# Kernel optimization log

Hardware: AMD Instinct MI355X
Metric: run time of the kernel (lower is better)

## Reference

```python
import jax, jax.numpy as jnp
import numpy as np

NUM_SEGMENTS = 128  # number of graphs (index.max()+1)


def setup_inputs() -> dict:
    key = jax.random.key(0)
    k1, k2, k3 = jax.random.split(key, 3)
    N, F, T, S, B = 200000, 3, 32, 32, NUM_SEGMENTS
    x = jax.random.normal(k1, (N, F), dtype=jnp.float32)
    v = jax.random.normal(k2, (F, T), dtype=jnp.float32)
    # lin exactly as in the module: linspace(-r, r, bump_steps).view(-1,1,1)
    lin = jnp.linspace(-1.1, 1.1, S, dtype=jnp.float32).reshape(S, 1, 1)
    index = jnp.sort(jax.random.randint(k3, (N,), 0, B, dtype=jnp.int64))
    return {"x": x, "index": index, "v": v, "lin": lin, "scale": 500}


def reference(x, index, v, lin, scale):
    # nh: node heights [N, T]
    nh = x @ v
    # ecc: [S, N, T] broadcasted sigmoid bump
    ecc = jax.nn.sigmoid(scale * (lin - nh))
    # scatter-add over nodes into per-graph bins, then movedim(0,1):
    # segment_sum over leading axis after transposing to [N, S, T]
    # gives [B, S, T] directly (== index_add over dim 1 then movedim).
    out = jax.ops.segment_sum(jnp.transpose(ecc, (1, 0, 2)), index,
                              num_segments=NUM_SEGMENTS)
    return out
```

## Files before the change

kernel.cpp:

```cpp
#include <hip/hip_runtime.h>

#define NSEG 128
#define SSTEPS 32
#define TDIM 32
#define NG 8
#define DROWS 35
#define SPB 8
#define CSTR (DROWS * TDIM)
#define THREADS 256

__global__ __launch_bounds__(THREADS) void ect_kernel(
    const float* __restrict__ x,
    const int*   __restrict__ idx,
    const float* __restrict__ v,
    const float* __restrict__ lin,
    const int*   __restrict__ scale_p,
    float*       __restrict__ out,
    int N)
{
    __shared__ float d[NG][DROWS][TDIM];
    __shared__ float4 xs[NG][32];
    __shared__ int s_bounds[2];

    const int tid = threadIdx.x;
    const unsigned bx = blockIdx.x;
    const int b = bx >> 3;
    const int j = bx & (SPB - 1);

    if (tid < 64) {
        const int L = tid & 31;
        const int h = tid >> 5;
        const int target = b + h;
        const int g0 = (int)(((long long)target * N) >> 7);

        const int hi_last = idx[N - 1];
        int p1 = g0 - 1024 + 64 * L;
        int pc1 = min(max(p1, 0), N - 1);
        int val32 = idx[pc1];
        const bool is64 = (hi_last == 0);
        int val = is64 ? idx[2 * pc1] : val32;

        bool pred1 = (p1 < 0) ? true : ((p1 >= N) ? false : (val < target));
        unsigned long long m1 = __ballot(pred1);
        unsigned hm1 = (unsigned)(m1 >> (h * 32));

        if (hm1 == 0u || hm1 == 0xFFFFFFFFu) {
            if (L == 0) {
                int lo = 0, hi = N;
                while (lo < hi) {
                    int mid = (lo + hi) >> 1;
                    int vv = is64 ? idx[2 * mid] : idx[mid];
                    if (vv < target) lo = mid + 1; else hi = mid;
                }
                s_bounds[h] = lo;
            }
        } else {
            const int A = g0 - 1024 + 64 * (31 - __builtin_clz(hm1));
            int p2 = A + 1 + 2 * L;
            int pc2 = min(max(p2, 0), N - 1);
            int v2 = is64 ? idx[2 * pc2] : idx[pc2];
            bool pred2 = (p2 < 0) ? true : ((p2 >= N) ? false : (v2 < target));
            unsigned long long m2 = __ballot(pred2);
            unsigned hm2 = (unsigned)(m2 >> (h * 32));
            const int B = hm2 ? (A + 1 + 2 * (31 - __builtin_clz(hm2))) : A;
            int p3 = B + 1;
            int pc3 = min(p3, N - 1);
            int v3 = is64 ? idx[2 * pc3] : idx[pc3];
            bool pred3 = (p3 >= N) ? false : (v3 < target);
            if (L == 0) s_bounds[h] = pred3 ? (B + 2) : (B + 1);
        }
    } else {
        float4* dz = (float4*)d;
        for (int i = tid - 64; i < NG * CSTR / 4; i += THREADS - 64)
            dz[i] = make_float4(0.f, 0.f, 0.f, 0.f);
    }

    const float lin0 = lin[0];
    const float step = lin[1] - lin0;
    const float inv_step = 1.0f / step;
    const float negl0 = -lin0 * inv_step;
    const float scale = (float)scale_p[0];
    const float zstep = scale * step;

    const int t = tid & 31;
    const int g = tid >> 5;
    const float v0 = v[t], v1 = v[TDIM + t], v2 = v[2 * TDIM + t];
    float* dg = &d[g][0][t];

    __syncthreads();

    const int start = s_bounds[0], end = s_bounds[1];
    const int cnt_n = end - start;
    const int chunk = (cnt_n + SPB - 1) / SPB;
    const int k0 = start + j * chunk;
    const int k1 = min(k0 + chunk, end);

    {
        const int span = k1 - k0;
        const int cg = (span > 0) ? ((span + NG - 1) >> 3) : 0;
        const int kg0 = k0 + g * cg;
        const int kg1 = min(kg0 + cg, k1);
        float4* xsg = &xs[g][0];
        float cnt = 0.f;

        for (int kb = kg0; kb < kg1; kb += 32) {
            const int nb = min(32, kg1 - kb);
            if (t < nb) {
                const float* xp = x + (size_t)(kb + t) * 3;
                xsg[t] = make_float4(xp[0], xp[1], xp[2], 0.f);
            }
            float4 cur = xsg[0];
            for (int r = 0; r < nb; ++r) {
                const float4 nxt = xsg[min(r + 1, nb - 1)];

                const float nh = fmaf(cur.x, v0, fmaf(cur.y, v1, cur.z * v2));
                float u = fmaf(nh, inv_step, negl0);
                u = fminf(fmaxf(u, -2.0f), 34.0f);
                const float rf = rintf(u);
                if (rf < 32.0f) {
                    if (rf <= -2.0f) cnt += 1.0f;
                    else {
                        const float E = __expf((rf - u) * zstep);
                        const float a = E * __builtin_amdgcn_rcpf(1.0f + E);
                        const int row = (int)rf + 2;
                        float* p = dg + row * 32;
                        const float a0 = p[0];
                        const float a1 = p[32];
                        p[0]  = a0 + a;
                        p[32] = a1 + (1.0f - a);
                    }
                }
                cur = nxt;
            }
        }
        dg[0] = cnt;
    }
    __syncthreads();

    {
        float4* c0 = (float4*)d;
        for (int i = tid; i < CSTR / 4; i += THREADS) {
            float4 a = c0[i];
            #pragma unroll
            for (int gg = 1; gg < NG; ++gg) {
                const float4 bq = ((const float4*)((const float*)d + gg * CSTR))[i];
                a.x += bq.x; a.y += bq.y; a.z += bq.z; a.w += bq.w;
            }
            c0[i] = a;
        }
    }
    __syncthreads();

    {
        float* df = (float*)d;
        float* sums = (float*)xs;
        const int rb = tid >> 5;
        const int rowb = 2 + rb * 4;
        float w0 = df[(rowb + 0) * 32 + t];
        float w1 = df[(rowb + 1) * 32 + t];
        float w2 = df[(rowb + 2) * 32 + t];
        float w3 = df[(rowb + 3) * 32 + t];
        w1 += w0; w2 += w1; w3 += w2;
        sums[rb * 32 + t] = w3;
        __syncthreads();
        float off = df[t] + df[32 + t];
        #pragma unroll
        for (int r = 0; r < 8; ++r) {
            const float sv = sums[r * 32 + t];
            off += (r < rb) ? sv : 0.f;
        }
        df[(rowb + 0) * 32 + t] = w0 + off;
        df[(rowb + 1) * 32 + t] = w1 + off;
        df[(rowb + 2) * 32 + t] = w2 + off;
        df[(rowb + 3) * 32 + t] = w3 + off;
    }
    __syncthreads();

    {
        const float* df = (const float*)d;
        float* ob = out + (size_t)b * (SSTEPS * TDIM);
        #pragma unroll
        for (int q = 0; q < 4; ++q)
            atomicAdd(&ob[q * 256 + tid], df[64 + q * 256 + tid]);
    }
}

extern "C" void kernel_launch(void* const* d_in, const int* in_sizes, int n_in,
                              void* d_out, int out_size, void* d_ws, size_t ws_size,
                              hipStream_t stream) {
    const float* x     = (const float*)d_in[0];
    const int*   index = (const int*)d_in[1];
    const float* v     = (const float*)d_in[2];
    const float* lin   = (const float*)d_in[3];
    const int*   scale = (const int*)d_in[4];
    float* out = (float*)d_out;
    const int N = in_sizes[0] / 3;

    hipMemsetAsync(d_out, 0, (size_t)out_size * sizeof(float), stream);
    ect_kernel<<<NSEG * SPB, THREADS, 0, stream>>>(x, index, v, lin, scale, out, N);
}
```

Baseline: 71.91 us.

## Unroll node loop by four branchless and widen boundary search to full wavefronts

The per-node accumulation loop is unrolled by four, and the control flow is replaced by predicated weights that go to a dummy row, so four exp/rcp computations can be interleaved before the LDS read-modify-writes. The segment boundary search now uses one 64-lane wavefront per bound with a ballot-and-popcount second stage, and it short-circuits the first and last segments. The aim is to raise instruction-level parallelism in the hot loop and cut latency in the prologue. In exchange, every node now pays for the exp even when it falls outside the bump range, and the zeroing loop has fewer threads.

After: 72.12 us. Within noise of the previous version (+0.3%).

```diff
diff --git a/kernel.cpp b/kernel.cpp
--- a/kernel.cpp
+++ b/kernel.cpp
@@ -27,51 +27,48 @@
     const int b = bx >> 3;
     const int j = bx & (SPB - 1);
 
-    if (tid < 64) {
-        const int L = tid & 31;
-        const int h = tid >> 5;
-        const int target = b + h;
-        const int g0 = (int)(((long long)target * N) >> 7);
-
-        const int hi_last = idx[N - 1];
-        int p1 = g0 - 1024 + 64 * L;
-        int pc1 = min(max(p1, 0), N - 1);
-        int val32 = idx[pc1];
-        const bool is64 = (hi_last == 0);
-        int val = is64 ? idx[2 * pc1] : val32;
-
-        bool pred1 = (p1 < 0) ? true : ((p1 >= N) ? false : (val < target));
-        unsigned long long m1 = __ballot(pred1);
-        unsigned hm1 = (unsigned)(m1 >> (h * 32));
-
-        if (hm1 == 0u || hm1 == 0xFFFFFFFFu) {
-            if (L == 0) {
-                int lo = 0, hi = N;
-                while (lo < hi) {
-                    int mid = (lo + hi) >> 1;
-                    int vv = is64 ? idx[2 * mid] : idx[mid];
-                    if (vv < target) lo = mid + 1; else hi = mid;
+    if (tid < 128) {
+        const int w = tid >> 6;
+        const int L = tid & 63;
+        const int target = b + w;
+        if (target == 0) {
+            if (L == 0) s_bounds[0] = 0;
+        } else if (target == NSEG) {
+            if (L == 0) s_bounds[1] = N;
+        } else {
+            const int g0 = (int)(((long long)target * N) >> 7);
+            const int hi_last = idx[N - 1];
+            const bool is64 = (hi_last == 0);
+
+            const int p1 = g0 - 1024 + 32 * L;
+            const int pc1 = min(max(p1, 0), N - 1);
+            const int val = is64 ? idx[2 * pc1] : idx[pc1];
+            const bool pred1 = (p1 < 0) ? true : ((p1 >= N) ? false : (val < target));
+            const unsigned long long m1 = __ballot(pred1);
+
+            if (m1 == 0ull || ~m1 == 0ull) {
+                if (L == 0) {
+                    int lo = 0, hi = N;
+                    while (lo < hi) {
+                        int mid = (lo + hi) >> 1;
+                        int vv = is64 ? idx[2 * mid] : idx[mid];
+                        if (vv < target) lo = mid + 1; else hi = mid;
+                    }
+                    s_bounds[w] = lo;
                 }
-                s_bounds[h] = lo;
-            }
-        } else {
-            const int A = g0 - 1024 + 64 * (31 - __builtin_clz(hm1));
-            int p2 = A + 1 + 2 * L;
-            int pc2 = min(max(p2, 0), N - 1);
-            int v2 = is64 ? idx[2 * pc2] : idx[pc2];
-            bool pred2 = (p2 < 0) ? true : ((p2 >= N) ? false : (v2 < target));
-            unsigned long long m2 = __ballot(pred2);
-            unsigned hm2 = (unsigned)(m2 >> (h * 32));
-            const int B = hm2 ? (A + 1 + 2 * (31 - __builtin_clz(hm2))) : A;
-            int p3 = B + 1;
-            int pc3 = min(p3, N - 1);
-            int v3 = is64 ? idx[2 * pc3] : idx[pc3];
-            bool pred3 = (p3 >= N) ? false : (v3 < target);
-            if (L == 0) s_bounds[h] = pred3 ? (B + 2) : (B + 1);
+            } else {
+                const int A = g0 - 1024 + 32 * (63 - __builtin_clzll(m1));
+                const int p2 = A + 1 + L;
+                const int pc2 = min(p2, N - 1);
+                const int v2 = is64 ? idx[2 * pc2] : idx[pc2];
+                const bool pred2 = (p2 >= N) ? false : (v2 < target);
+                const unsigned long long m2 = __ballot(pred2);
+                if (L == 0) s_bounds[w] = A + 1 + __popcll(m2);
+            }
         }
     } else {
         float4* dz = (float4*)d;
-        for (int i = tid - 64; i < NG * CSTR / 4; i += THREADS - 64)
+        for (int i = tid - 128; i < NG * CSTR / 4; i += THREADS - 128)
             dz[i] = make_float4(0.f, 0.f, 0.f, 0.f);
     }
 
@@ -103,34 +100,54 @@
         float4* xsg = &xs[g][0];
         float cnt = 0.f;
 
+        auto wcalc = [&](const float4 c, const bool valid,
+                         float& wA, float& wB, int& row) {
+            const float nh = fmaf(c.x, v0, fmaf(c.y, v1, c.z * v2));
+            const float u = fminf(fmaxf(fmaf(nh, inv_step, negl0), -2.0f), 34.0f);
+            const float rf = rintf(u);
+            const float E = __expf((rf - u) * zstep);
+            const float a = E * __builtin_amdgcn_rcpf(1.0f + E);
+            const bool lv = valid & (rf > -2.0f) & (rf < 32.0f);
+            cnt += (valid & (rf <= -2.0f)) ? 1.0f : 0.0f;
+            row = lv ? ((int)rf + 2) : 1;
+            wA = lv ? a : 0.f;
+            wB = lv ? (1.0f - a) : 0.f;
+        };
+
         for (int kb = kg0; kb < kg1; kb += 32) {
             const int nb = min(32, kg1 - kb);
             if (t < nb) {
                 const float* xp = x + (size_t)(kb + t) * 3;
                 xsg[t] = make_float4(xp[0], xp[1], xp[2], 0.f);
             }
-            float4 cur = xsg[0];
-            for (int r = 0; r < nb; ++r) {
-                const float4 nxt = xsg[min(r + 1, nb - 1)];
-
-                const float nh = fmaf(cur.x, v0, fmaf(cur.y, v1, cur.z * v2));
-                float u = fmaf(nh, inv_step, negl0);
-                u = fminf(fmaxf(u, -2.0f), 34.0f);
-                const float rf = rintf(u);
-                if (rf < 32.0f) {
-                    if (rf <= -2.0f) cnt += 1.0f;
-                    else {
-                        const float E = __expf((rf - u) * zstep);
-                        const float a = E * __builtin_amdgcn_rcpf(1.0f + E);
-                        const int row = (int)rf + 2;
-                        float* p = dg + row * 32;
-                        const float a0 = p[0];
-                        const float a1 = p[32];
-                        p[0]  = a0 + a;
-                        p[32] = a1 + (1.0f - a);
-                    }
-                }
-                cur = nxt;
+            float4 c0 = xsg[0];
+            float4 c1 = xsg[min(1, nb - 1)];
+            float4 c2 = xsg[min(2, nb - 1)];
+            float4 c3 = xsg[min(3, nb - 1)];
+            for (int r = 0; r < nb; r += 4) {
+                const int rn = r + 4;
+                const float4 n0 = xsg[min(rn,     nb - 1)];
+                const float4 n1 = xsg[min(rn + 1, nb - 1)];
+                const float4 n2 = xsg[min(rn + 2, nb - 1)];
+                const float4 n3 = xsg[min(rn + 3, nb - 1)];
+
+                float wA0, wB0, wA1, wB1, wA2, wB2, wA3, wB3;
+                int row0, row1, row2, row3;
+                wcalc(c0, r + 0 < nb, wA0, wB0, row0);
+                wcalc(c1, r + 1 < nb, wA1, wB1, row1);
+                wcalc(c2, r + 2 < nb, wA2, wB2, row2);
+                wcalc(c3, r + 3 < nb, wA3, wB3, row3);
+
+                { float* p = dg + row0 * 32; const float a0 = p[0], a1 = p[32];
+                  p[0] = a0 + wA0; p[32] = a1 + wB0; }
+                { float* p = dg + row1 * 32; const float a0 = p[0], a1 = p[32];
+                  p[0] = a0 + wA1; p[32] = a1 + wB1; }
+                { float* p = dg + row2 * 32; const float a0 = p[0], a1 = p[32];
+                  p[0] = a0 + wA2; p[32] = a1 + wB2; }
+                { float* p = dg + row3 * 32; const float a0 = p[0], a1 = p[32];
+                  p[0] = a0 + wA3; p[32] = a1 + wB3; }
+
+                c0 = n0; c1 = n1; c2 = n2; c3 = n3;
             }
         }
         dg[0] = cnt;
```
